# Optimization experiments

Hardware: AMD Instinct MI355X
Metric: run time of the kernel (lower is better)

Reference implementation:

```python
import jax, jax.numpy as jnp
import numpy as np

N_POINTS = 1_000_000
NUM_SEGMENTS = 100_000
D_IN = 64
FEA_COMPRE = 16  # linear: 64 -> 2*fea_compre = 32


def setup_inputs() -> dict:
    key = jax.random.key(0)
    k1, k2, k3, k4, k5 = jax.random.split(key, 5)
    shuffled_ind = jax.random.permutation(k1, N_POINTS)  # shuffle of point rows
    pt_gfeatures = jax.random.normal(k2, (N_POINTS, D_IN), dtype=jnp.float32)
    pt_localfeatures2 = jax.random.normal(k3, (N_POINTS, D_IN), dtype=jnp.float32)
    pt_inv = jnp.sort(jax.random.randint(k4, (N_POINTS,), 0, NUM_SEGMENTS))
    W = jax.random.normal(k5, (D_IN, 2 * FEA_COMPRE), dtype=jnp.float32) * (1.0 / np.sqrt(D_IN))
    b = jnp.zeros((2 * FEA_COMPRE,), dtype=jnp.float32)
    return {
        "shuffled_ind": shuffled_ind,
        "pt_gfeatures": pt_gfeatures,
        "pt_localfeatures2": pt_localfeatures2,
        "pt_inv": pt_inv,
        "W": W,
        "b": b,
    }


def reference(shuffled_ind, pt_gfeatures, pt_localfeatures2, pt_inv, W, b):
    # gather + add fused expression: [N, 64]
    x = pt_gfeatures[shuffled_ind, :] + pt_localfeatures2
    # scatter_max over segments: [M, 64]
    pooled = jax.ops.segment_max(x, pt_inv, num_segments=NUM_SEGMENTS)
    # empty segments come back as -inf; torch_scatter leaves them at fill value -> use 0
    pooled = jnp.where(jnp.isfinite(pooled), pooled, jnp.zeros((), pooled.dtype))
    # fea_compre*2 = 32 is in (0, 64), so the compression branch runs
    return jax.nn.relu(pooled @ W + b)  # [M, 32]
```

## Files before the change

kernel.cpp:

```cpp
#include <hip/hip_runtime.h>
#include <hip/hip_bf16.h>
#include <math.h>


#define D_IN 64
#define K_OUT 32
#define WAVES_PER_BLOCK 4

__global__ __launch_bounds__(256) void seg_starts_kernel(
    const int* __restrict__ pt_inv, int n, int* __restrict__ starts, int M)
{
    int s = blockIdx.x * blockDim.x + threadIdx.x;
    if (s > M) return;
    int lo = 0, hi = n;
    while (lo < hi) {
        int mid = (lo + hi) >> 1;
        if (pt_inv[mid] < s) lo = mid + 1; else hi = mid;
    }
    starts[s] = lo;
}

__global__ __launch_bounds__(64 * WAVES_PER_BLOCK) void pool_gemm_kernel(
    const int*   __restrict__ shuffled_ind,
    const float* __restrict__ g,
    const float* __restrict__ l,
    const int*   __restrict__ starts,
    const float* __restrict__ W,
    const float* __restrict__ b,
    float*       __restrict__ out,
    int M)
{
    __shared__ float Ws[D_IN * K_OUT];
    __shared__ float bs[K_OUT];
    __shared__ float pool[WAVES_PER_BLOCK][D_IN];

    const int tid = threadIdx.x;
    for (int i = tid; i < D_IN * K_OUT; i += 64 * WAVES_PER_BLOCK) Ws[i] = W[i];
    if (tid < K_OUT) bs[tid] = b[tid];

    const int wid  = tid >> 6;
    const int lane = tid & 63;
    const int s    = blockIdx.x * WAVES_PER_BLOCK + wid;
    const bool active = (s < M);

    float m = -INFINITY;
    if (active) {
        const int p0 = starts[s];
        const int p1 = starts[s + 1];
        for (int p = p0; p < p1; ++p) {
            const int ind = shuffled_ind[p];
            const float x = g[(size_t)ind * D_IN + lane] + l[(size_t)p * D_IN + lane];
            m = fmaxf(m, x);
        }
        if (p1 <= p0) m = 0.0f;
    }

    if (active) pool[wid][lane] = m;
    __syncthreads();

    if (active && lane < K_OUT) {
        float acc = bs[lane];
        #pragma unroll
        for (int c = 0; c < D_IN; ++c) {
            acc = fmaf(pool[wid][c], Ws[c * K_OUT + lane], acc);
        }
        out[(size_t)s * K_OUT + lane] = fmaxf(acc, 0.0f);
    }
}

extern "C" void kernel_launch(void* const* d_in, const int* in_sizes, int n_in,
                              void* d_out, int out_size, void* d_ws, size_t ws_size,
                              hipStream_t stream)
{
    const int*   shuffled_ind = (const int*)  d_in[0];
    const float* g            = (const float*)d_in[1];
    const float* l            = (const float*)d_in[2];
    const int*   pt_inv       = (const int*)  d_in[3];
    const float* W            = (const float*)d_in[4];
    const float* b            = (const float*)d_in[5];
    float*       out          = (float*)d_out;

    const int N = in_sizes[0];
    const int M = out_size / K_OUT;

    int* starts = (int*)d_ws;

    {
        int threads = 256;
        int blocks  = (M + 1 + threads - 1) / threads;
        seg_starts_kernel<<<blocks, threads, 0, stream>>>(pt_inv, N, starts, M);
    }
    {
        int blocks = (M + WAVES_PER_BLOCK - 1) / WAVES_PER_BLOCK;
        pool_gemm_kernel<<<blocks, 64 * WAVES_PER_BLOCK, 0, stream>>>(
            shuffled_ind, g, l, starts, W, b, out, M);
    }
}
```

Baseline: 167.6 us.

## Replace per-segment pooling with row-chunked scan using order-preserving atomicMax

Each wave now scans a fixed chunk of 128 sorted rows instead of one segment, with indices and segment ids staged in LDS and 8 gathers unrolled per step to keep more loads in flight. Segments that lie fully inside a chunk are written directly. Segments crossing chunk boundaries are merged with atomicMax on an order-preserving unsigned encoding of float in a workspace buffer, which is first filled with an encoded -inf. A separate GEMM kernel then decodes the pooled rows, maps empty segments to zero and applies the linear layer and ReLU. This removes the binary-search pass and the load imbalance from uneven segment sizes, at the cost of an extra 25.6 MB pooled buffer that must be initialised, written and re-read, plus two more kernel launches.

```diff
diff --git a/kernel.cpp b/kernel.cpp
--- a/kernel.cpp
+++ b/kernel.cpp
@@ -5,7 +5,119 @@
 
 #define D_IN 64
 #define K_OUT 32
-#define WAVES_PER_BLOCK 4
+#define RPW 128
+#define WPB 4
+#define ENC_NEG_INF 0x007FFFFFu
+
+__device__ __forceinline__ unsigned enc_f32(float f) {
+    unsigned u = __float_as_uint(f);
+    return (u & 0x80000000u) ? ~u : (u | 0x80000000u);
+}
+__device__ __forceinline__ float dec_f32(unsigned u) {
+    unsigned b = (u & 0x80000000u) ? (u ^ 0x80000000u) : ~u;
+    return __uint_as_float(b);
+}
+
+__global__ __launch_bounds__(256) void init_pooled_kernel(uint4* __restrict__ p, int n4)
+{
+    const uint4 v = make_uint4(ENC_NEG_INF, ENC_NEG_INF, ENC_NEG_INF, ENC_NEG_INF);
+    for (int i = blockIdx.x * blockDim.x + threadIdx.x; i < n4; i += gridDim.x * blockDim.x)
+        p[i] = v;
+}
+
+__global__ __launch_bounds__(64 * WPB) void scan_max_kernel(
+    const int*   __restrict__ shuffled_ind,
+    const float* __restrict__ g,
+    const float* __restrict__ l,
+    const int*   __restrict__ pt_inv,
+    unsigned*    __restrict__ pooled,
+    int n)
+{
+    __shared__ int ind_lds[WPB][RPW];
+    __shared__ int seg_lds[WPB][RPW];
+
+    const int tid  = threadIdx.x;
+    const int wid  = tid >> 6;
+    const int lane = tid & 63;
+    const int base = (blockIdx.x * WPB + wid) * RPW;
+    const int rows = min(RPW, n - base);
+
+    #pragma unroll
+    for (int j0 = 0; j0 < RPW; j0 += 64) {
+        const int r = j0 + lane;
+        if (r < rows) {
+            ind_lds[wid][r] = shuffled_ind[base + r];
+            seg_lds[wid][r] = pt_inv[base + r];
+        }
+    }
+    __syncthreads();
+    if (rows <= 0) return;
+
+    int   curSeg   = seg_lds[wid][0];
+    int   segFirst = 0;
+    float m        = -INFINITY;
+
+    for (int i0 = 0; i0 < rows; i0 += 8) {
+        float x[8];
+        #pragma unroll
+        for (int k = 0; k < 8; ++k) {
+            const int i  = min(i0 + k, rows - 1);
+            const int ind = ind_lds[wid][i];
+            x[k] = g[(size_t)ind * D_IN + lane] + l[(size_t)(base + i) * D_IN + lane];
+        }
+        #pragma unroll
+        for (int k = 0; k < 8; ++k) {
+            const int i = i0 + k;
+            if (i < rows) {
+                const int seg = seg_lds[wid][i];
+                if (seg != curSeg) {
+                    unsigned* p = pooled + (size_t)curSeg * D_IN + lane;
+                    const unsigned e = enc_f32(m);
+                    if (segFirst == 0) atomicMax(p, e); else *p = e;
+                    curSeg = seg; segFirst = i; m = x[k];
+                } else {
+                    m = fmaxf(m, x[k]);
+                }
+            }
+        }
+    }
+    atomicMax(pooled + (size_t)curSeg * D_IN + lane, enc_f32(m));
+}
+
+__global__ __launch_bounds__(256) void gemm_kernel(
+    const unsigned* __restrict__ pooled,
+    const float*    __restrict__ W,
+    const float*    __restrict__ b,
+    float*          __restrict__ out,
+    int M)
+{
+    __shared__ float Ws[D_IN * K_OUT];
+    __shared__ float bs[K_OUT];
+    __shared__ float pool[WPB][D_IN];
+
+    const int tid = threadIdx.x;
+    for (int i = tid; i < D_IN * K_OUT; i += 64 * WPB) Ws[i] = W[i];
+    if (tid < K_OUT) bs[tid] = b[tid];
+
+    const int wid  = tid >> 6;
+    const int lane = tid & 63;
+    const int s    = blockIdx.x * WPB + wid;
+    const bool active = (s < M);
+
+    if (active) {
+        const unsigned u = pooled[(size_t)s * D_IN + lane];
+        pool[wid][lane] = (u == ENC_NEG_INF) ? 0.0f : dec_f32(u);
+    }
+    __syncthreads();
+
+    if (active && lane < K_OUT) {
+        float acc = bs[lane];
+        #pragma unroll
+        for (int c = 0; c < D_IN; ++c)
+            acc = fmaf(pool[wid][c], Ws[c * K_OUT + lane], acc);
+        out[(size_t)s * K_OUT + lane] = fmaxf(acc, 0.0f);
+    }
+}
 
 __global__ __launch_bounds__(256) void seg_starts_kernel(
     const int* __restrict__ pt_inv, int n, int* __restrict__ starts, int M)
@@ -13,57 +125,40 @@
     int s = blockIdx.x * blockDim.x + threadIdx.x;
     if (s > M) return;
     int lo = 0, hi = n;
-    while (lo < hi) {
-        int mid = (lo + hi) >> 1;
-        if (pt_inv[mid] < s) lo = mid + 1; else hi = mid;
-    }
+    while (lo < hi) { int mid = (lo + hi) >> 1; if (pt_inv[mid] < s) lo = mid + 1; else hi = mid; }
     starts[s] = lo;
 }
 
-__global__ __launch_bounds__(64 * WAVES_PER_BLOCK) void pool_gemm_kernel(
-    const int*   __restrict__ shuffled_ind,
-    const float* __restrict__ g,
-    const float* __restrict__ l,
-    const int*   __restrict__ starts,
-    const float* __restrict__ W,
-    const float* __restrict__ b,
-    float*       __restrict__ out,
-    int M)
+__global__ __launch_bounds__(256) void pool_gemm_kernel(
+    const int* __restrict__ shuffled_ind, const float* __restrict__ g,
+    const float* __restrict__ l, const int* __restrict__ starts,
+    const float* __restrict__ W, const float* __restrict__ b,
+    float* __restrict__ out, int M)
 {
     __shared__ float Ws[D_IN * K_OUT];
     __shared__ float bs[K_OUT];
-    __shared__ float pool[WAVES_PER_BLOCK][D_IN];
-
+    __shared__ float pool[WPB][D_IN];
     const int tid = threadIdx.x;
-    for (int i = tid; i < D_IN * K_OUT; i += 64 * WAVES_PER_BLOCK) Ws[i] = W[i];
+    for (int i = tid; i < D_IN * K_OUT; i += 64 * WPB) Ws[i] = W[i];
     if (tid < K_OUT) bs[tid] = b[tid];
-
-    const int wid  = tid >> 6;
-    const int lane = tid & 63;
-    const int s    = blockIdx.x * WAVES_PER_BLOCK + wid;
+    const int wid = tid >> 6, lane = tid & 63;
+    const int s = blockIdx.x * WPB + wid;
     const bool active = (s < M);
-
     float m = -INFINITY;
     if (active) {
-        const int p0 = starts[s];
-        const int p1 = starts[s + 1];
+        const int p0 = starts[s], p1 = starts[s + 1];
         for (int p = p0; p < p1; ++p) {
             const int ind = shuffled_ind[p];
-            const float x = g[(size_t)ind * D_IN + lane] + l[(size_t)p * D_IN + lane];
-            m = fmaxf(m, x);
+            m = fmaxf(m, g[(size_t)ind * D_IN + lane] + l[(size_t)p * D_IN + lane]);
         }
         if (p1 <= p0) m = 0.0f;
     }
-
     if (active) pool[wid][lane] = m;
     __syncthreads();
-
     if (active && lane < K_OUT) {
         float acc = bs[lane];
         #pragma unroll
-        for (int c = 0; c < D_IN; ++c) {
-            acc = fmaf(pool[wid][c], Ws[c * K_OUT + lane], acc);
-        }
+        for (int c = 0; c < D_IN; ++c) acc = fmaf(pool[wid][c], Ws[c * K_OUT + lane], acc);
         out[(size_t)s * K_OUT + lane] = fmaxf(acc, 0.0f);
     }
 }
@@ -83,16 +178,34 @@
     const int N = in_sizes[0];
     const int M = out_size / K_OUT;
 
-    int* starts = (int*)d_ws;
-
-    {
-        int threads = 256;
-        int blocks  = (M + 1 + threads - 1) / threads;
-        seg_starts_kernel<<<blocks, threads, 0, stream>>>(pt_inv, N, starts, M);
-    }
-    {
-        int blocks = (M + WAVES_PER_BLOCK - 1) / WAVES_PER_BLOCK;
-        pool_gemm_kernel<<<blocks, 64 * WAVES_PER_BLOCK, 0, stream>>>(
-            shuffled_ind, g, l, starts, W, b, out, M);
-    }
-}
+    const size_t pooled_bytes = (size_t)M * D_IN * sizeof(unsigned);
+
+    if (ws_size >= pooled_bytes) {
+        unsigned* pooled = (unsigned*)d_ws;
+        {
+            const int n4 = (int)(pooled_bytes / 16);
+            init_pooled_kernel<<<512, 256, 0, stream>>>((uint4*)pooled, n4);
+        }
+        {
+            const int rows_per_block = WPB * RPW;
+            const int blocks = (N + rows_per_block - 1) / rows_per_block;
+            scan_max_kernel<<<blocks, 64 * WPB, 0, stream>>>(
+                shuffled_ind, g, l, pt_inv, pooled, N);
+        }
+        {
+            const int blocks = (M + WPB - 1) / WPB;
+            gemm_kernel<<<blocks, 64 * WPB, 0, stream>>>(pooled, W, b, out, M);
+        }
+    } else {
+        int* starts = (int*)d_ws;
+        {
+            const int blocks = (M + 1 + 255) / 256;
+            seg_starts_kernel<<<blocks, 256, 0, stream>>>(pt_inv, N, starts, M);
+        }
+        {
+            const int blocks = (M + WPB - 1) / WPB;
+            pool_gemm_kernel<<<blocks, 64 * WPB, 0, stream>>>(
+                shuffled_ind, g, l, starts, W, b, out, M);
+        }
+    }
+}
```

Measured after the change: 179.9 us. 7.3% more time.
